# Performance work log

Hardware: AMD Instinct MI355X
Metric: run time of the kernel (lower is better)

## Reference

```python
import jax, jax.numpy as jnp
import numpy as np

EMB_SZ = 1024
NUM_HEADS = 16
HEAD_SIZE = EMB_SZ // NUM_HEADS  # 64; inputs must have last dim == HEAD_SIZE (module quirk)
B, S = 2, 2048


def setup_inputs() -> dict:
    key = jax.random.key(0)
    ks = jax.random.split(key, 8)
    return {
        "inputs_for_keys": jax.random.normal(ks[0], (B, S, HEAD_SIZE), jnp.float32),
        "inputs_for_values": jax.random.normal(ks[1], (B, S, HEAD_SIZE), jnp.float32),
        "inputs_for_queries": jax.random.normal(ks[2], (B, S, HEAD_SIZE), jnp.float32),
        # per-head projection weights, stacked over heads (glorot-ish scale)
        "Wk": jax.random.normal(ks[3], (NUM_HEADS, HEAD_SIZE, HEAD_SIZE), jnp.float32) * 0.125,
        "Wv": jax.random.normal(ks[4], (NUM_HEADS, HEAD_SIZE, HEAD_SIZE), jnp.float32) * 0.125,
        "Wq": jax.random.normal(ks[5], (NUM_HEADS, HEAD_SIZE, HEAD_SIZE), jnp.float32) * 0.125,
        "Wo": jax.random.normal(ks[6], (EMB_SZ, EMB_SZ), jnp.float32) * 0.03,
        "bo": jnp.zeros((EMB_SZ,), jnp.float32),
    }


def reference(inputs_for_keys, inputs_for_values, inputs_for_queries, Wk, Wv, Wq, Wo, bo):
    # Each head sees the SAME full inputs (module quirk), distinct weights per head.
    K = jnp.einsum('bsd,hde->bhse', inputs_for_keys, Wk)      # [B,H,Sk,hs]
    V = jnp.einsum('bsd,hde->bhse', inputs_for_values, Wv)    # [B,H,Sk,hs]
    Q = jnp.einsum('bsd,hde->bhse', inputs_for_queries, Wq)   # [B,H,Sq,hs]

    Sq, Sk = Q.shape[2], K.shape[2]
    scores = jnp.einsum('bhqe,bhke->bhqk', Q, K)              # [B,H,Sq,Sk]
    # causal additive mask: -inf strictly above the diagonal (as in np.triu(..., k=1))
    mask = jnp.triu(jnp.full((Sq, Sk), -jnp.inf, dtype=scores.dtype), k=1)
    scale = jnp.asarray(Sk, scores.dtype) ** 0.5
    # NOTE: original divides AFTER adding the mask; -inf/scale == -inf so math matches
    attn = jax.nn.softmax((scores + mask) / scale, axis=-1)   # [B,H,Sq,Sk]

    heads = jnp.einsum('bhqk,bhke->bhqe', attn, V)            # [B,H,Sq,hs]
    # concat heads along last dim (head order matches the Python-loop concat)
    concat = heads.transpose(0, 2, 1, 3).reshape(heads.shape[0], Sq, -1)  # [B,Sq,emb]
    return concat @ Wo + bo                                   # Dense(emb_sz), linear activation
```

## Files before the change

### kernel.cpp

```cpp
#include <hip/hip_runtime.h>
#include <hip/hip_bf16.h>
#include <cstdint>

typedef unsigned short u16;
typedef __bf16 bf16x8 __attribute__((ext_vector_type(8)));
typedef u16 u16x8 __attribute__((ext_vector_type(8)));
typedef unsigned u32x4 __attribute__((ext_vector_type(4)));
typedef float f32x4 __attribute__((ext_vector_type(4)));
typedef float f32x16 __attribute__((ext_vector_type(16)));

#define B_ 2
#define S_ 2048
#define H_ 16
#define HS_ 64
#define EMB_ 1024
#define QSCALE 0.022097086912079608f
#define LOG2E  1.4426950408889634f

static __device__ __forceinline__ u16 f2bf(float f) {
  unsigned int u = __float_as_uint(f);
  u += 0x7fffu + ((u >> 16) & 1u);
  return (u16)(u >> 16);
}

static __device__ __forceinline__ float ex2(float x) {
#if __has_builtin(__builtin_amdgcn_exp2f)
  return __builtin_amdgcn_exp2f(x);
#else
  float r; asm("v_exp_f32 %0, %1" : "=v"(r) : "v"(x)); return r;
#endif
}

static __device__ __forceinline__ f32x4 mfma16(u16x8 a, u16x8 b, f32x4 c) {
  return __builtin_amdgcn_mfma_f32_16x16x32_bf16(
      __builtin_bit_cast(bf16x8, a), __builtin_bit_cast(bf16x8, b), c, 0, 0, 0);
}
static __device__ __forceinline__ f32x16 mfma32(u16x8 a, u16x8 b, f32x16 c) {
  return __builtin_amdgcn_mfma_f32_32x32x16_bf16(
      __builtin_bit_cast(bf16x8, a), __builtin_bit_cast(bf16x8, b), c, 0, 0, 0);
}

static __device__ __forceinline__ char* swzb(void* base, int row, int colbyte) {
  return (char*)base + ((row * 128 + colbyte) ^ ((row & 7) << 4));
}
static __device__ __forceinline__ u16x8* swzp(void* base, int row, int colbyte) {
  return (u16x8*)swzb(base, row, colbyte);
}

static __device__ __forceinline__ void pk_swap(float a0, float a1, float b0, float b1,
                                               unsigned& x, unsigned& y) {
  unsigned A, Bv;
  asm("v_cvt_pk_bf16_f32 %0, %1, %2" : "=v"(A) : "v"(a0), "v"(a1));
  asm("v_cvt_pk_bf16_f32 %0, %1, %2" : "=v"(Bv) : "v"(b0), "v"(b1));
  asm("v_permlane32_swap_b32 %0, %1" : "+v"(A), "+v"(Bv));
  x = A; y = Bv;
}

__global__ __launch_bounds__(256) void k_transpose_wo(const float* __restrict__ Wo,
                                                      u16* __restrict__ Wot) {
  __shared__ __align__(16) u16 T[64][72];
  const int kb = blockIdx.y * 64, nb = blockIdx.x * 64;
  const int r = threadIdx.x >> 2;
  const int c0 = (threadIdx.x & 3) << 4;
  const float* src = Wo + (size_t)(kb + r) * EMB_ + nb + c0;
#pragma unroll
  for (int i = 0; i < 16; i += 4) {
    float4 f = *(const float4*)(src + i);
    T[c0 + i + 0][r] = f2bf(f.x);
    T[c0 + i + 1][r] = f2bf(f.y);
    T[c0 + i + 2][r] = f2bf(f.z);
    T[c0 + i + 3][r] = f2bf(f.w);
  }
  __syncthreads();
  u16* dst = Wot + (size_t)(nb + r) * EMB_ + kb + c0;
  *(u16x8*)(dst)     = *(const u16x8*)&T[r][c0];
  *(u16x8*)(dst + 8) = *(const u16x8*)&T[r][c0 + 8];
}

__global__ __launch_bounds__(256) void k_proj(
    const float* __restrict__ xq, const float* __restrict__ xk, const float* __restrict__ xv,
    const float* __restrict__ Wq, const float* __restrict__ Wk, const float* __restrict__ Wv,
    u16* __restrict__ Qf, u16* __restrict__ Kf, u16* __restrict__ Vf) {
  __shared__ __align__(16) u16 Xb[64][64];
  __shared__ __align__(16) u16 Wb[64][64];
  __shared__ __align__(16) u16 Tt[64][64];
  const int sb = blockIdx.x;
  const int bh = blockIdx.y;
  const int b = bh >> 4, h = bh & 15;
  const int t = threadIdx.x;
  const int r = t >> 2, c0 = (t & 3) << 4;
  const int lane = t & 63, wv = t >> 6;
  const int lq = lane & 15, lg = lane >> 4;
  const int l31 = lane & 31, hi = lane >> 5;
  const float* xs[3] = {xq, xk, xv};
  const float* ws3[3] = {Wq, Wk, Wv};

  for (int tn = 0; tn < 3; ++tn) {
    __syncthreads();
    const float* src = xs[tn] + ((size_t)(b * S_ + sb * 64 + r)) * HS_ + c0;
#pragma unroll
    for (int i = 0; i < 16; i += 8) {
      float4 fa = *(const float4*)(src + i);
      float4 fb = *(const float4*)(src + i + 4);
      u16x8 v = {f2bf(fa.x), f2bf(fa.y), f2bf(fa.z), f2bf(fa.w),
                 f2bf(fb.x), f2bf(fb.y), f2bf(fb.z), f2bf(fb.w)};
      *swzp(Xb, r, (c0 + i) * 2) = v;
    }
    const float* wsp = ws3[tn] + ((size_t)(h * HS_ + r)) * HS_ + c0;
#pragma unroll
    for (int i = 0; i < 16; i += 4) {
      float4 f = *(const float4*)(wsp + i);
      *(u16*)swzb(Wb, c0 + i + 0, r * 2) = f2bf(f.x);
      *(u16*)swzb(Wb, c0 + i + 1, r * 2) = f2bf(f.y);
      *(u16*)swzb(Wb, c0 + i + 2, r * 2) = f2bf(f.z);
      *(u16*)swzb(Wb, c0 + i + 3, r * 2) = f2bf(f.w);
    }
    __syncthreads();
    if (tn < 2) {
      u16x8 a0 = *swzp(Xb, wv * 16 + lq, lg * 16);
      u16x8 a1 = *swzp(Xb, wv * 16 + lq, 64 + lg * 16);
      const float osc = (tn == 0) ? (QSCALE * LOG2E) : 1.0f;
#pragma unroll
      for (int et = 0; et < 4; ++et) {
        u16x8 b0 = *swzp(Wb, et * 16 + lq, lg * 16);
        u16x8 b1 = *swzp(Wb, et * 16 + lq, 64 + lg * 16);
        f32x4 acc = {0.f, 0.f, 0.f, 0.f};
        acc = mfma16(a0, b0, acc);
        acc = mfma16(a1, b1, acc);
#pragma unroll
        for (int rr = 0; rr < 4; ++rr)
          *(u16*)swzb(Tt, wv * 16 + lg * 4 + rr, (et * 16 + lq) * 2) = f2bf(acc[rr] * osc);
      }
    } else {
      u16x8 xb0 = *swzp(Xb, wv * 16 + lq, lg * 16);
      u16x8 xb1 = *swzp(Xb, wv * 16 + lq, 64 + lg * 16);
#pragma unroll
      for (int et = 0; et < 4; ++et) {
        u16x8 a0 = *swzp(Wb, et * 16 + lq, lg * 16);
        u16x8 a1 = *swzp(Wb, et * 16 + lq, 64 + lg * 16);
        f32x4 acc = {0.f, 0.f, 0.f, 0.f};
        acc = mfma16(a0, xb0, acc);
        acc = mfma16(a1, xb1, acc);
#pragma unroll
        for (int rr = 0; rr < 4; ++rr)
          *(u16*)swzb(Tt, et * 16 + lg * 4 + rr, (wv * 16 + lq) * 2) = f2bf(acc[rr]);
      }
    }
    __syncthreads();
    if (tn < 2) {
      u16* dst = (tn == 0) ? Qf : Kf;
#pragma unroll
      for (int tl = 0; tl < 2; ++tl) {
        u16x8 v = *swzp(Tt, tl * 32 + l31, wv * 32 + hi * 16);
        size_t off = (((size_t)(bh * 64 + sb * 2 + tl)) * 4 + wv) * 512 + lane * 8;
        *(u16x8*)(dst + off) = v;
      }
    } else {
#pragma unroll
      for (int eta = 0; eta < 2; ++eta) {
        u16x8 v = *swzp(Tt, eta * 32 + l31, wv * 32 + hi * 16);
        size_t off = ((((size_t)(bh * 32 + sb)) * 2 + eta) * 4 + wv) * 512 + lane * 8;
        *(u16x8*)(Vf + off) = v;
      }
    }
  }
}

__global__ __launch_bounds__(128) void k_attn(
    const u16* __restrict__ Qf, const u16* __restrict__ Kf, const u16* __restrict__ Vf,
    u16* __restrict__ Co) {
  __shared__ float Xch[64][33];
  __shared__ __align__(16) u16 Osw[32][64];
  const int bid = blockIdx.x;
  const int xcd = bid & 7, idx = bid >> 3;
  const int bh = (xcd << 2) | (idx & 3);
  const int t = 63 - (idx >> 2);
  const int b = bh >> 4, h = bh & 15;
  const int w = threadIdx.x >> 6;
  const int l = threadIdx.x & 63;
  const int lq = l & 31, hi = l >> 5;
  const int qg = t * 32 + lq;
  const int n = (t >> 1) + 1;
  const int mid = n >> 1;
  const int jbeg = w ? mid : 0;
  const int jhot = w ? (n - 1) : mid;
  const float NEG = -3.0e38f;

  const u16* Qbase = Qf + (((size_t)(bh * 64 + t)) * 4) * 512 + l * 8;
  const u16* Kbase = Kf + ((size_t)(bh * 64) * 4) * 512 + l * 8;
  const u16* Vbase = Vf + ((size_t)(bh * 32) * 8) * 512 + l * 8;

  u16x8 qf[4];
#pragma unroll
  for (int ss = 0; ss < 4; ++ss) qf[ss] = *(const u16x8*)(Qbase + ss * 512);

  f32x16 o0, o1;
#pragma unroll
  for (int r = 0; r < 16; ++r) { o0[r] = 0.f; o1[r] = 0.f; }
  float ll = 0.f;

  u16x8 kl[4], kh[4], vl[4], vh[4];
  {
    const u16* p = Kbase + (size_t)jbeg * 8 * 512;
#pragma unroll
    for (int ss = 0; ss < 4; ++ss) {
      kl[ss] = *(const u16x8*)(p + ss * 512);
      kh[ss] = *(const u16x8*)(p + (4 + ss) * 512);
    }
  }

  for (int j = jbeg; j < jhot; ++j) {
    const u16* pv = Vbase + (size_t)j * 8 * 512;
#pragma unroll
    for (int kp = 0; kp < 4; ++kp) {
      vl[kp] = *(const u16x8*)(pv + kp * 512);
      vh[kp] = *(const u16x8*)(pv + (4 + kp) * 512);
    }
    f32x16 s0, s1;
#pragma unroll
    for (int r = 0; r < 16; ++r) { s0[r] = -16.f; s1[r] = -16.f; }
    __builtin_amdgcn_s_setprio(1);
    s0 = mfma32(kl[0], qf[0], s0);
    s0 = mfma32(kl[1], qf[1], s0);
    s0 = mfma32(kl[2], qf[2], s0);
    s0 = mfma32(kl[3], qf[3], s0);
    s1 = mfma32(kh[0], qf[0], s1);
    s1 = mfma32(kh[1], qf[1], s1);
    s1 = mfma32(kh[2], qf[2], s1);
    s1 = mfma32(kh[3], qf[3], s1);
    __builtin_amdgcn_s_setprio(0);
    {
      const u16* pk = Kbase + (size_t)(j + 1) * 8 * 512;
#pragma unroll
      for (int ss = 0; ss < 4; ++ss) {
        kl[ss] = *(const u16x8*)(pk + ss * 512);
        kh[ss] = *(const u16x8*)(pk + (4 + ss) * 512);
      }
    }
    float ps = 0.f;
#pragma unroll
    for (int r = 0; r < 16; ++r) { s0[r] = ex2(s0[r]); ps += s0[r]; }
#pragma unroll
    for (int r = 0; r < 16; ++r) { s1[r] = ex2(s1[r]); ps += s1[r]; }
    ll += ps;
    u16x8 pf0, pf1, pf2, pf3;
    {
      unsigned w0, w1, w2, w3;
      pk_swap(s0[0], s0[1], s0[4], s0[5], w0, w2);
      pk_swap(s0[2], s0[3], s0[6], s0[7], w1, w3);
      pf0 = __builtin_bit_cast(u16x8, (u32x4){w0, w1, w2, w3});
      pk_swap(s0[8], s0[9], s0[12], s0[13], w0, w2);
      pk_swap(s0[10], s0[11], s0[14], s0[15], w1, w3);
      pf1 = __builtin_bit_cast(u16x8, (u32x4){w0, w1, w2, w3});
      pk_swap(s1[0], s1[1], s1[4], s1[5], w0, w2);
      pk_swap(s1[2], s1[3], s1[6], s1[7], w1, w3);
      pf2 = __builtin_bit_cast(u16x8, (u32x4){w0, w1, w2, w3});
      pk_swap(s1[8], s1[9], s1[12], s1[13], w0, w2);
      pk_swap(s1[10], s1[11], s1[14], s1[15], w1, w3);
      pf3 = __builtin_bit_cast(u16x8, (u32x4){w0, w1, w2, w3});
    }
    __builtin_amdgcn_s_setprio(1);
    o0 = mfma32(vl[0], pf0, o0);
    o1 = mfma32(vh[0], pf0, o1);
    o0 = mfma32(vl[1], pf1, o0);
    o1 = mfma32(vh[1], pf1, o1);
    o0 = mfma32(vl[2], pf2, o0);
    o1 = mfma32(vh[2], pf2, o1);
    o0 = mfma32(vl[3], pf3, o0);
    o1 = mfma32(vh[3], pf3, o1);
    __builtin_amdgcn_s_setprio(0);
  }

  if (w) {
    const int j = n - 1;
    const u16* pv = Vbase + (size_t)j * 8 * 512;
#pragma unroll
    for (int kp = 0; kp < 4; ++kp) {
      vl[kp] = *(const u16x8*)(pv + kp * 512);
      vh[kp] = *(const u16x8*)(pv + (4 + kp) * 512);
    }
    f32x16 s0, s1;
#pragma unroll
    for (int r = 0; r < 16; ++r) { s0[r] = -16.f; s1[r] = -16.f; }
    s0 = mfma32(kl[0], qf[0], s0);
    s0 = mfma32(kl[1], qf[1], s0);
    s0 = mfma32(kl[2], qf[2], s0);
    s0 = mfma32(kl[3], qf[3], s0);
    if (t & 1) {
      s1 = mfma32(kh[0], qf[0], s1);
      s1 = mfma32(kh[1], qf[1], s1);
      s1 = mfma32(kh[2], qf[2], s1);
      s1 = mfma32(kh[3], qf[3], s1);
    }
    if (t & 1) {
#pragma unroll
      for (int r = 0; r < 16; ++r) {
        int kv = j * 64 + 32 + (r & 3) + 8 * (r >> 2) + 4 * hi;
        if (kv > qg) s1[r] = NEG;
      }
    } else {
#pragma unroll
      for (int r = 0; r < 16; ++r) {
        int kv = j * 64 + (r & 3) + 8 * (r >> 2) + 4 * hi;
        if (kv > qg) s0[r] = NEG;
      }
    }
    float ps = 0.f;
#pragma unroll
    for (int r = 0; r < 16; ++r) { s0[r] = ex2(s0[r]); ps += s0[r]; }
    if (t & 1) {
#pragma unroll
      for (int r = 0; r < 16; ++r) { s1[r] = ex2(s1[r]); ps += s1[r]; }
    }
    ll += ps;
    u16x8 pf0, pf1, pf2, pf3;
    {
      unsigned w0, w1, w2, w3;
      pk_swap(s0[0], s0[1], s0[4], s0[5], w0, w2);
      pk_swap(s0[2], s0[3], s0[6], s0[7], w1, w3);
      pf0 = __builtin_bit_cast(u16x8, (u32x4){w0, w1, w2, w3});
      pk_swap(s0[8], s0[9], s0[12], s0[13], w0, w2);
      pk_swap(s0[10], s0[11], s0[14], s0[15], w1, w3);
      pf1 = __builtin_bit_cast(u16x8, (u32x4){w0, w1, w2, w3});
      if (t & 1) {
        pk_swap(s1[0], s1[1], s1[4], s1[5], w0, w2);
        pk_swap(s1[2], s1[3], s1[6], s1[7], w1, w3);
        pf2 = __builtin_bit_cast(u16x8, (u32x4){w0, w1, w2, w3});
        pk_swap(s1[8], s1[9], s1[12], s1[13], w0, w2);
        pk_swap(s1[10], s1[11], s1[14], s1[15], w1, w3);
        pf3 = __builtin_bit_cast(u16x8, (u32x4){w0, w1, w2, w3});
      }
    }
    o0 = mfma32(vl[0], pf0, o0);
    o1 = mfma32(vh[0], pf0, o1);
    o0 = mfma32(vl[1], pf1, o0);
    o1 = mfma32(vh[1], pf1, o1);
    if (t & 1) {
      o0 = mfma32(vl[2], pf2, o0);
      o1 = mfma32(vh[2], pf2, o1);
      o0 = mfma32(vl[3], pf3, o0);
      o1 = mfma32(vh[3], pf3, o1);
    }
#pragma unroll
    for (int r = 0; r < 16; ++r) { Xch[l][r] = o0[r]; Xch[l][16 + r] = o1[r]; }
    Xch[l][32] = ll;
  }
  __syncthreads();
  if (w == 0) {
#pragma unroll
    for (int r = 0; r < 16; ++r) { o0[r] += Xch[l][r]; o1[r] += Xch[l][16 + r]; }
    ll += Xch[l][32];
    ll += __shfl_xor(ll, 32);
    float inv = 1.0f / ll;
#pragma unroll
    for (int r = 0; r < 16; ++r) {
      int drow = (r & 3) + 8 * (r >> 2) + 4 * hi;
      *(u16*)swzb(Osw, lq, drow * 2) = f2bf(o0[r] * inv);
      *(u16*)swzb(Osw, lq, (32 + drow) * 2) = f2bf(o1[r] * inv);
    }
    u16* dst = Co + ((size_t)(b * S_ + qg)) * EMB_ + h * HS_ + hi * 32;
#pragma unroll
    for (int k = 0; k < 4; ++k) {
      u16x8 vv = *swzp(Osw, lq, (hi * 32 + k * 8) * 2);
      *(u16x8*)(dst + k * 8) = vv;
    }
  }
}

__global__ __launch_bounds__(256) void k_outproj(
    const u16* __restrict__ Cc, const u16* __restrict__ Wot,
    const float* __restrict__ bo, float* __restrict__ out) {
  __shared__ __align__(16) u16 As[64][64];
  __shared__ __align__(16) u16 Bs[128][64];
  const int bid = blockIdx.x;
  const int xcd = bid & 7, sl = bid >> 3;
  const int mb = (xcd << 3) | (sl >> 3);
  const int nb = sl & 7;
  const int t = threadIdx.x;
  const int lane = t & 63, wv = t >> 6;
  const int lq = lane & 15, lg = lane >> 4;
  const int wr = wv >> 1, wc = wv & 1;
  const int srA = t >> 2, scA = (t & 3) << 4;
  const int srB = t >> 1, scB = (t & 1) << 5;
  f32x4 acc[2][4];
#pragma unroll
  for (int mi = 0; mi < 2; ++mi)
#pragma unroll
    for (int ni = 0; ni < 4; ++ni) { f32x4 z = {0.f, 0.f, 0.f, 0.f}; acc[mi][ni] = z; }
  const u16* abase = Cc + ((size_t)(mb * 64 + srA)) * EMB_ + scA;
  const u16* bbase = Wot + ((size_t)(nb * 128 + srB)) * EMB_ + scB;
  u16x8 ar[2], br[4];
#pragma unroll
  for (int q = 0; q < 2; ++q) ar[q] = *(const u16x8*)(abase + q * 8);
#pragma unroll
  for (int q = 0; q < 4; ++q) br[q] = *(const u16x8*)(bbase + q * 8);
  for (int kt = 0; kt < 16; ++kt) {
    __syncthreads();
#pragma unroll
    for (int q = 0; q < 2; ++q) *swzp(As, srA, (scA + q * 8) * 2) = ar[q];
#pragma unroll
    for (int q = 0; q < 4; ++q) *swzp(Bs, srB, (scB + q * 8) * 2) = br[q];
    __syncthreads();
    if (kt < 15) {
#pragma unroll
      for (int q = 0; q < 2; ++q) ar[q] = *(const u16x8*)(abase + (kt + 1) * 64 + q * 8);
#pragma unroll
      for (int q = 0; q < 4; ++q) br[q] = *(const u16x8*)(bbase + (kt + 1) * 64 + q * 8);
    }
#pragma unroll
    for (int kf = 0; kf < 2; ++kf) {
      u16x8 af[2], bf[4];
#pragma unroll
      for (int mi = 0; mi < 2; ++mi)
        af[mi] = *swzp(As, wr * 32 + mi * 16 + lq, kf * 64 + lg * 16);
#pragma unroll
      for (int ni = 0; ni < 4; ++ni)
        bf[ni] = *swzp(Bs, wc * 64 + ni * 16 + lq, kf * 64 + lg * 16);
#pragma unroll
      for (int mi = 0; mi < 2; ++mi)
#pragma unroll
        for (int ni = 0; ni < 4; ++ni)
          acc[mi][ni] = mfma16(af[mi], bf[ni], acc[mi][ni]);
    }
  }
#pragma unroll
  for (int mi = 0; mi < 2; ++mi) {
#pragma unroll
    for (int ni = 0; ni < 4; ++ni) {
      int col = nb * 128 + wc * 64 + ni * 16 + lq;
      float bv = bo[col];
#pragma unroll
      for (int rr = 0; rr < 4; ++rr) {
        int row = mb * 64 + wr * 32 + mi * 16 + lg * 4 + rr;
        out[(size_t)row * EMB_ + col] = acc[mi][ni][rr] + bv;
      }
    }
  }
}

extern "C" void kernel_launch(void* const* d_in, const int* in_sizes, int n_in,
                              void* d_out, int out_size, void* d_ws, size_t ws_size,
                              hipStream_t stream) {
  const float* xk = (const float*)d_in[0];
  const float* xv = (const float*)d_in[1];
  const float* xq = (const float*)d_in[2];
  const float* Wk = (const float*)d_in[3];
  const float* Wv = (const float*)d_in[4];
  const float* Wq = (const float*)d_in[5];
  const float* Wo = (const float*)d_in[6];
  const float* bo = (const float*)d_in[7];
  float* out = (float*)d_out;
  char* ws = (char*)d_ws;
  const size_t MB8 = (size_t)8 * 1024 * 1024;
  u16* Qfw = (u16*)(ws);
  u16* Kfw = (u16*)(ws + MB8);
  u16* Vfw = (u16*)(ws + 2 * MB8);
  u16* Cw  = (u16*)(ws + 3 * MB8);
  u16* Wot = (u16*)(ws + 4 * MB8);

  k_transpose_wo<<<dim3(16, 16), 256, 0, stream>>>(Wo, Wot);
  k_proj<<<dim3(32, 32), 256, 0, stream>>>(xq, xk, xv, Wq, Wk, Wv, Qfw, Kfw, Vfw);
  k_attn<<<2048, 128, 0, stream>>>(Qfw, Kfw, Vfw, Cw);
  k_outproj<<<512, 256, 0, stream>>>(Cw, Wot, bo, out);
}
```

Before: 71.73 us.

## Pair causal query tiles per attention block, split projection grid, prefetch V

The projection kernel now spreads Q, K and V over a third grid dimension, so it runs one tensor per block instead of looping over three. The attention kernel processes two query tiles per block (t and 63-t) to balance causal work, and halves the grid. It also prefetches V one step ahead alongside K, uses a tree reduction for the row sums, and adds a launch-bounds occupancy hint. Costs are more register pressure from the V double-buffering, and a longer serial run per block.

After: 65.34 us. 8.9% less time.

```diff
diff --git a/kernel.cpp b/kernel.cpp
--- a/kernel.cpp
+++ b/kernel.cpp
@@ -29,6 +29,16 @@
 #else
   float r; asm("v_exp_f32 %0, %1" : "=v"(r) : "v"(x)); return r;
 #endif
+}
+
+static __device__ __forceinline__ float tsum16(const f32x16& s) {
+  float a0 = s[0] + s[1],  a1 = s[2] + s[3];
+  float a2 = s[4] + s[5],  a3 = s[6] + s[7];
+  float a4 = s[8] + s[9],  a5 = s[10] + s[11];
+  float a6 = s[12] + s[13], a7 = s[14] + s[15];
+  a0 += a1; a2 += a3; a4 += a5; a6 += a7;
+  a0 += a2; a4 += a6;
+  return a0 + a4;
 }
 
 static __device__ __forceinline__ f32x4 mfma16(u16x8 a, u16x8 b, f32x4 c) {
@@ -86,87 +96,85 @@
   __shared__ __align__(16) u16 Tt[64][64];
   const int sb = blockIdx.x;
   const int bh = blockIdx.y;
+  const int tn = blockIdx.z;
   const int b = bh >> 4, h = bh & 15;
   const int t = threadIdx.x;
   const int r = t >> 2, c0 = (t & 3) << 4;
   const int lane = t & 63, wv = t >> 6;
   const int lq = lane & 15, lg = lane >> 4;
   const int l31 = lane & 31, hi = lane >> 5;
-  const float* xs[3] = {xq, xk, xv};
-  const float* ws3[3] = {Wq, Wk, Wv};
-
-  for (int tn = 0; tn < 3; ++tn) {
-    __syncthreads();
-    const float* src = xs[tn] + ((size_t)(b * S_ + sb * 64 + r)) * HS_ + c0;
-#pragma unroll
-    for (int i = 0; i < 16; i += 8) {
-      float4 fa = *(const float4*)(src + i);
-      float4 fb = *(const float4*)(src + i + 4);
-      u16x8 v = {f2bf(fa.x), f2bf(fa.y), f2bf(fa.z), f2bf(fa.w),
-                 f2bf(fb.x), f2bf(fb.y), f2bf(fb.z), f2bf(fb.w)};
-      *swzp(Xb, r, (c0 + i) * 2) = v;
-    }
-    const float* wsp = ws3[tn] + ((size_t)(h * HS_ + r)) * HS_ + c0;
-#pragma unroll
-    for (int i = 0; i < 16; i += 4) {
-      float4 f = *(const float4*)(wsp + i);
-      *(u16*)swzb(Wb, c0 + i + 0, r * 2) = f2bf(f.x);
-      *(u16*)swzb(Wb, c0 + i + 1, r * 2) = f2bf(f.y);
-      *(u16*)swzb(Wb, c0 + i + 2, r * 2) = f2bf(f.z);
-      *(u16*)swzb(Wb, c0 + i + 3, r * 2) = f2bf(f.w);
-    }
-    __syncthreads();
-    if (tn < 2) {
-      u16x8 a0 = *swzp(Xb, wv * 16 + lq, lg * 16);
-      u16x8 a1 = *swzp(Xb, wv * 16 + lq, 64 + lg * 16);
-      const float osc = (tn == 0) ? (QSCALE * LOG2E) : 1.0f;
-#pragma unroll
-      for (int et = 0; et < 4; ++et) {
-        u16x8 b0 = *swzp(Wb, et * 16 + lq, lg * 16);
-        u16x8 b1 = *swzp(Wb, et * 16 + lq, 64 + lg * 16);
-        f32x4 acc = {0.f, 0.f, 0.f, 0.f};
-        acc = mfma16(a0, b0, acc);
-        acc = mfma16(a1, b1, acc);
-#pragma unroll
-        for (int rr = 0; rr < 4; ++rr)
-          *(u16*)swzb(Tt, wv * 16 + lg * 4 + rr, (et * 16 + lq) * 2) = f2bf(acc[rr] * osc);
-      }
-    } else {
-      u16x8 xb0 = *swzp(Xb, wv * 16 + lq, lg * 16);
-      u16x8 xb1 = *swzp(Xb, wv * 16 + lq, 64 + lg * 16);
-#pragma unroll
-      for (int et = 0; et < 4; ++et) {
-        u16x8 a0 = *swzp(Wb, et * 16 + lq, lg * 16);
-        u16x8 a1 = *swzp(Wb, et * 16 + lq, 64 + lg * 16);
-        f32x4 acc = {0.f, 0.f, 0.f, 0.f};
-        acc = mfma16(a0, xb0, acc);
-        acc = mfma16(a1, xb1, acc);
-#pragma unroll
-        for (int rr = 0; rr < 4; ++rr)
-          *(u16*)swzb(Tt, et * 16 + lg * 4 + rr, (wv * 16 + lq) * 2) = f2bf(acc[rr]);
-      }
-    }
-    __syncthreads();
-    if (tn < 2) {
-      u16* dst = (tn == 0) ? Qf : Kf;
-#pragma unroll
-      for (int tl = 0; tl < 2; ++tl) {
-        u16x8 v = *swzp(Tt, tl * 32 + l31, wv * 32 + hi * 16);
-        size_t off = (((size_t)(bh * 64 + sb * 2 + tl)) * 4 + wv) * 512 + lane * 8;
-        *(u16x8*)(dst + off) = v;
-      }
-    } else {
-#pragma unroll
-      for (int eta = 0; eta < 2; ++eta) {
-        u16x8 v = *swzp(Tt, eta * 32 + l31, wv * 32 + hi * 16);
-        size_t off = ((((size_t)(bh * 32 + sb)) * 2 + eta) * 4 + wv) * 512 + lane * 8;
-        *(u16x8*)(Vf + off) = v;
-      }
-    }
-  }
-}
-
-__global__ __launch_bounds__(128) void k_attn(
+  const float* xs = (tn == 0) ? xq : (tn == 1) ? xk : xv;
+  const float* wsp3 = (tn == 0) ? Wq : (tn == 1) ? Wk : Wv;
+
+  const float* src = xs + ((size_t)(b * S_ + sb * 64 + r)) * HS_ + c0;
+#pragma unroll
+  for (int i = 0; i < 16; i += 8) {
+    float4 fa = *(const float4*)(src + i);
+    float4 fb = *(const float4*)(src + i + 4);
+    u16x8 v = {f2bf(fa.x), f2bf(fa.y), f2bf(fa.z), f2bf(fa.w),
+               f2bf(fb.x), f2bf(fb.y), f2bf(fb.z), f2bf(fb.w)};
+    *swzp(Xb, r, (c0 + i) * 2) = v;
+  }
+  const float* wsp = wsp3 + ((size_t)(h * HS_ + r)) * HS_ + c0;
+#pragma unroll
+  for (int i = 0; i < 16; i += 4) {
+    float4 f = *(const float4*)(wsp + i);
+    *(u16*)swzb(Wb, c0 + i + 0, r * 2) = f2bf(f.x);
+    *(u16*)swzb(Wb, c0 + i + 1, r * 2) = f2bf(f.y);
+    *(u16*)swzb(Wb, c0 + i + 2, r * 2) = f2bf(f.z);
+    *(u16*)swzb(Wb, c0 + i + 3, r * 2) = f2bf(f.w);
+  }
+  __syncthreads();
+  if (tn < 2) {
+    u16x8 a0 = *swzp(Xb, wv * 16 + lq, lg * 16);
+    u16x8 a1 = *swzp(Xb, wv * 16 + lq, 64 + lg * 16);
+    const float osc = (tn == 0) ? (QSCALE * LOG2E) : 1.0f;
+#pragma unroll
+    for (int et = 0; et < 4; ++et) {
+      u16x8 b0 = *swzp(Wb, et * 16 + lq, lg * 16);
+      u16x8 b1 = *swzp(Wb, et * 16 + lq, 64 + lg * 16);
+      f32x4 acc = {0.f, 0.f, 0.f, 0.f};
+      acc = mfma16(a0, b0, acc);
+      acc = mfma16(a1, b1, acc);
+#pragma unroll
+      for (int rr = 0; rr < 4; ++rr)
+        *(u16*)swzb(Tt, wv * 16 + lg * 4 + rr, (et * 16 + lq) * 2) = f2bf(acc[rr] * osc);
+    }
+  } else {
+    u16x8 xb0 = *swzp(Xb, wv * 16 + lq, lg * 16);
+    u16x8 xb1 = *swzp(Xb, wv * 16 + lq, 64 + lg * 16);
+#pragma unroll
+    for (int et = 0; et < 4; ++et) {
+      u16x8 a0 = *swzp(Wb, et * 16 + lq, lg * 16);
+      u16x8 a1 = *swzp(Wb, et * 16 + lq, 64 + lg * 16);
+      f32x4 acc = {0.f, 0.f, 0.f, 0.f};
+      acc = mfma16(a0, xb0, acc);
+      acc = mfma16(a1, xb1, acc);
+#pragma unroll
+      for (int rr = 0; rr < 4; ++rr)
+        *(u16*)swzb(Tt, et * 16 + lg * 4 + rr, (wv * 16 + lq) * 2) = f2bf(acc[rr]);
+    }
+  }
+  __syncthreads();
+  if (tn < 2) {
+    u16* dst = (tn == 0) ? Qf : Kf;
+#pragma unroll
+    for (int tl = 0; tl < 2; ++tl) {
+      u16x8 v = *swzp(Tt, tl * 32 + l31, wv * 32 + hi * 16);
+      size_t off = (((size_t)(bh * 64 + sb * 2 + tl)) * 4 + wv) * 512 + lane * 8;
+      *(u16x8*)(dst + off) = v;
+    }
+  } else {
+#pragma unroll
+    for (int eta = 0; eta < 2; ++eta) {
+      u16x8 v = *swzp(Tt, eta * 32 + l31, wv * 32 + hi * 16);
+      size_t off = ((((size_t)(bh * 32 + sb)) * 2 + eta) * 4 + wv) * 512 + lane * 8;
+      *(u16x8*)(Vf + off) = v;
+    }
+  }
+}
+
+__global__ __launch_bounds__(128, 2) void k_attn(
     const u16* __restrict__ Qf, const u16* __restrict__ Kf, const u16* __restrict__ Vf,
     u16* __restrict__ Co) {
   __shared__ float Xch[64][33];
@@ -174,155 +182,83 @@
   const int bid = blockIdx.x;
   const int xcd = bid & 7, idx = bid >> 3;
   const int bh = (xcd << 2) | (idx & 3);
-  const int t = 63 - (idx >> 2);
+  const int pr = idx >> 2;
   const int b = bh >> 4, h = bh & 15;
   const int w = threadIdx.x >> 6;
   const int l = threadIdx.x & 63;
   const int lq = l & 31, hi = l >> 5;
-  const int qg = t * 32 + lq;
-  const int n = (t >> 1) + 1;
-  const int mid = n >> 1;
-  const int jbeg = w ? mid : 0;
-  const int jhot = w ? (n - 1) : mid;
   const float NEG = -3.0e38f;
 
-  const u16* Qbase = Qf + (((size_t)(bh * 64 + t)) * 4) * 512 + l * 8;
   const u16* Kbase = Kf + ((size_t)(bh * 64) * 4) * 512 + l * 8;
   const u16* Vbase = Vf + ((size_t)(bh * 32) * 8) * 512 + l * 8;
 
-  u16x8 qf[4];
-#pragma unroll
-  for (int ss = 0; ss < 4; ++ss) qf[ss] = *(const u16x8*)(Qbase + ss * 512);
-
-  f32x16 o0, o1;
-#pragma unroll
-  for (int r = 0; r < 16; ++r) { o0[r] = 0.f; o1[r] = 0.f; }
-  float ll = 0.f;
-
-  u16x8 kl[4], kh[4], vl[4], vh[4];
-  {
-    const u16* p = Kbase + (size_t)jbeg * 8 * 512;
-#pragma unroll
-    for (int ss = 0; ss < 4; ++ss) {
-      kl[ss] = *(const u16x8*)(p + ss * 512);
-      kh[ss] = *(const u16x8*)(p + (4 + ss) * 512);
-    }
-  }
-
-  for (int j = jbeg; j < jhot; ++j) {
-    const u16* pv = Vbase + (size_t)j * 8 * 512;
-#pragma unroll
-    for (int kp = 0; kp < 4; ++kp) {
-      vl[kp] = *(const u16x8*)(pv + kp * 512);
-      vh[kp] = *(const u16x8*)(pv + (4 + kp) * 512);
-    }
-    f32x16 s0, s1;
-#pragma unroll
-    for (int r = 0; r < 16; ++r) { s0[r] = -16.f; s1[r] = -16.f; }
-    __builtin_amdgcn_s_setprio(1);
-    s0 = mfma32(kl[0], qf[0], s0);
-    s0 = mfma32(kl[1], qf[1], s0);
-    s0 = mfma32(kl[2], qf[2], s0);
-    s0 = mfma32(kl[3], qf[3], s0);
-    s1 = mfma32(kh[0], qf[0], s1);
-    s1 = mfma32(kh[1], qf[1], s1);
-    s1 = mfma32(kh[2], qf[2], s1);
-    s1 = mfma32(kh[3], qf[3], s1);
-    __builtin_amdgcn_s_setprio(0);
+#pragma unroll 1
+  for (int ph = 0; ph < 2; ++ph) {
+    const int t = ph ? (63 - pr) : pr;
+    const int qg = t * 32 + lq;
+    const int n = (t >> 1) + 1;
+    const int mid = n >> 1;
+    const int jbeg = w ? mid : 0;
+    const int jhot = w ? (n - 1) : mid;
+
+    const u16* Qbase = Qf + (((size_t)(bh * 64 + t)) * 4) * 512 + l * 8;
+    u16x8 qf[4];
+#pragma unroll
+    for (int ss = 0; ss < 4; ++ss) qf[ss] = *(const u16x8*)(Qbase + ss * 512);
+
+    f32x16 o0, o1;
+#pragma unroll
+    for (int r = 0; r < 16; ++r) { o0[r] = 0.f; o1[r] = 0.f; }
+    float ll = 0.f;
+
+    u16x8 kl[4], kh[4], vl[4], vh[4];
     {
-      const u16* pk = Kbase + (size_t)(j + 1) * 8 * 512;
+      const u16* pk = Kbase + (size_t)jbeg * 8 * 512;
+      const u16* pv = Vbase + (size_t)jbeg * 8 * 512;
 #pragma unroll
       for (int ss = 0; ss < 4; ++ss) {
         kl[ss] = *(const u16x8*)(pk + ss * 512);
         kh[ss] = *(const u16x8*)(pk + (4 + ss) * 512);
-      }
-    }
-    float ps = 0.f;
-#pragma unroll
-    for (int r = 0; r < 16; ++r) { s0[r] = ex2(s0[r]); ps += s0[r]; }
-#pragma unroll
-    for (int r = 0; r < 16; ++r) { s1[r] = ex2(s1[r]); ps += s1[r]; }
-    ll += ps;
-    u16x8 pf0, pf1, pf2, pf3;
-    {
-      unsigned w0, w1, w2, w3;
-      pk_swap(s0[0], s0[1], s0[4], s0[5], w0, w2);
-      pk_swap(s0[2], s0[3], s0[6], s0[7], w1, w3);
-      pf0 = __builtin_bit_cast(u16x8, (u32x4){w0, w1, w2, w3});
-      pk_swap(s0[8], s0[9], s0[12], s0[13], w0, w2);
-      pk_swap(s0[10], s0[11], s0[14], s0[15], w1, w3);
-      pf1 = __builtin_bit_cast(u16x8, (u32x4){w0, w1, w2, w3});
-      pk_swap(s1[0], s1[1], s1[4], s1[5], w0, w2);
-      pk_swap(s1[2], s1[3], s1[6], s1[7], w1, w3);
-      pf2 = __builtin_bit_cast(u16x8, (u32x4){w0, w1, w2, w3});
-      pk_swap(s1[8], s1[9], s1[12], s1[13], w0, w2);
-      pk_swap(s1[10], s1[11], s1[14], s1[15], w1, w3);
-      pf3 = __builtin_bit_cast(u16x8, (u32x4){w0, w1, w2, w3});
-    }
-    __builtin_amdgcn_s_setprio(1);
-    o0 = mfma32(vl[0], pf0, o0);
-    o1 = mfma32(vh[0], pf0, o1);
-    o0 = mfma32(vl[1], pf1, o0);
-    o1 = mfma32(vh[1], pf1, o1);
-    o0 = mfma32(vl[2], pf2, o0);
-    o1 = mfma32(vh[2], pf2, o1);
-    o0 = mfma32(vl[3], pf3, o0);
-    o1 = mfma32(vh[3], pf3, o1);
-    __builtin_amdgcn_s_setprio(0);
-  }
-
-  if (w) {
-    const int j = n - 1;
-    const u16* pv = Vbase + (size_t)j * 8 * 512;
-#pragma unroll
-    for (int kp = 0; kp < 4; ++kp) {
-      vl[kp] = *(const u16x8*)(pv + kp * 512);
-      vh[kp] = *(const u16x8*)(pv + (4 + kp) * 512);
-    }
-    f32x16 s0, s1;
-#pragma unroll
-    for (int r = 0; r < 16; ++r) { s0[r] = -16.f; s1[r] = -16.f; }
-    s0 = mfma32(kl[0], qf[0], s0);
-    s0 = mfma32(kl[1], qf[1], s0);
-    s0 = mfma32(kl[2], qf[2], s0);
-    s0 = mfma32(kl[3], qf[3], s0);
-    if (t & 1) {
+        vl[ss] = *(const u16x8*)(pv + ss * 512);
+        vh[ss] = *(const u16x8*)(pv + (4 + ss) * 512);
+      }
+    }
+
+    for (int j = jbeg; j < jhot; ++j) {
+      f32x16 s0, s1;
+#pragma unroll
+      for (int r = 0; r < 16; ++r) { s0[r] = -16.f; s1[r] = -16.f; }
+      __builtin_amdgcn_s_setprio(1);
+      s0 = mfma32(kl[0], qf[0], s0);
+      s0 = mfma32(kl[1], qf[1], s0);
+      s0 = mfma32(kl[2], qf[2], s0);
+      s0 = mfma32(kl[3], qf[3], s0);
       s1 = mfma32(kh[0], qf[0], s1);
       s1 = mfma32(kh[1], qf[1], s1);
       s1 = mfma32(kh[2], qf[2], s1);
       s1 = mfma32(kh[3], qf[3], s1);
-    }
-    if (t & 1) {
-#pragma unroll
-      for (int r = 0; r < 16; ++r) {
-        int kv = j * 64 + 32 + (r & 3) + 8 * (r >> 2) + 4 * hi;
-        if (kv > qg) s1[r] = NEG;
-      }
-    } else {
-#pragma unroll
-      for (int r = 0; r < 16; ++r) {
-        int kv = j * 64 + (r & 3) + 8 * (r >> 2) + 4 * hi;
-        if (kv > qg) s0[r] = NEG;
-      }
-    }
-    float ps = 0.f;
-#pragma unroll
-    for (int r = 0; r < 16; ++r) { s0[r] = ex2(s0[r]); ps += s0[r]; }
-    if (t & 1) {
-#pragma unroll
-      for (int r = 0; r < 16; ++r) { s1[r] = ex2(s1[r]); ps += s1[r]; }
-    }
-    ll += ps;
-    u16x8 pf0, pf1, pf2, pf3;
-    {
-      unsigned w0, w1, w2, w3;
-      pk_swap(s0[0], s0[1], s0[4], s0[5], w0, w2);
-      pk_swap(s0[2], s0[3], s0[6], s0[7], w1, w3);
-      pf0 = __builtin_bit_cast(u16x8, (u32x4){w0, w1, w2, w3});
-      pk_swap(s0[8], s0[9], s0[12], s0[13], w0, w2);
-      pk_swap(s0[10], s0[11], s0[14], s0[15], w1, w3);
-      pf1 = __builtin_bit_cast(u16x8, (u32x4){w0, w1, w2, w3});
-      if (t & 1) {
+      __builtin_amdgcn_s_setprio(0);
+      {
+        const u16* pk = Kbase + (size_t)(j + 1) * 8 * 512;
+#pragma unroll
+        for (int ss = 0; ss < 4; ++ss) {
+          kl[ss] = *(const u16x8*)(pk + ss * 512);
+          kh[ss] = *(const u16x8*)(pk + (4 + ss) * 512);
+        }
+      }
+#pragma unroll
+      for (int r = 0; r < 16; ++r) s0[r] = ex2(s0[r]);
+#pragma unroll
+      for (int r = 0; r < 16; ++r) s1[r] = ex2(s1[r]);
+      u16x8 pf0, pf1, pf2, pf3;
+      {
+        unsigned w0, w1, w2, w3;
+        pk_swap(s0[0], s0[1], s0[4], s0[5], w0, w2);
+        pk_swap(s0[2], s0[3], s0[6], s0[7], w1, w3);
+        pf0 = __builtin_bit_cast(u16x8, (u32x4){w0, w1, w2, w3});
+        pk_swap(s0[8], s0[9], s0[12], s0[13], w0, w2);
+        pk_swap(s0[10], s0[11], s0[14], s0[15], w1, w3);
+        pf1 = __builtin_bit_cast(u16x8, (u32x4){w0, w1, w2, w3});
         pk_swap(s1[0], s1[1], s1[4], s1[5], w0, w2);
         pk_swap(s1[2], s1[3], s1[6], s1[7], w1, w3);
         pf2 = __builtin_bit_cast(u16x8, (u32x4){w0, w1, w2, w3});
@@ -330,40 +266,116 @@
         pk_swap(s1[10], s1[11], s1[14], s1[15], w1, w3);
         pf3 = __builtin_bit_cast(u16x8, (u32x4){w0, w1, w2, w3});
       }
-    }
-    o0 = mfma32(vl[0], pf0, o0);
-    o1 = mfma32(vh[0], pf0, o1);
-    o0 = mfma32(vl[1], pf1, o0);
-    o1 = mfma32(vh[1], pf1, o1);
-    if (t & 1) {
+      __builtin_amdgcn_s_setprio(1);
+      o0 = mfma32(vl[0], pf0, o0);
+      o1 = mfma32(vh[0], pf0, o1);
+      o0 = mfma32(vl[1], pf1, o0);
+      o1 = mfma32(vh[1], pf1, o1);
       o0 = mfma32(vl[2], pf2, o0);
       o1 = mfma32(vh[2], pf2, o1);
       o0 = mfma32(vl[3], pf3, o0);
       o1 = mfma32(vh[3], pf3, o1);
-    }
-#pragma unroll
-    for (int r = 0; r < 16; ++r) { Xch[l][r] = o0[r]; Xch[l][16 + r] = o1[r]; }
-    Xch[l][32] = ll;
-  }
-  __syncthreads();
-  if (w == 0) {
-#pragma unroll
-    for (int r = 0; r < 16; ++r) { o0[r] += Xch[l][r]; o1[r] += Xch[l][16 + r]; }
-    ll += Xch[l][32];
-    ll += __shfl_xor(ll, 32);
-    float inv = 1.0f / ll;
-#pragma unroll
-    for (int r = 0; r < 16; ++r) {
-      int drow = (r & 3) + 8 * (r >> 2) + 4 * hi;
-      *(u16*)swzb(Osw, lq, drow * 2) = f2bf(o0[r] * inv);
-      *(u16*)swzb(Osw, lq, (32 + drow) * 2) = f2bf(o1[r] * inv);
-    }
-    u16* dst = Co + ((size_t)(b * S_ + qg)) * EMB_ + h * HS_ + hi * 32;
-#pragma unroll
-    for (int k = 0; k < 4; ++k) {
-      u16x8 vv = *swzp(Osw, lq, (hi * 32 + k * 8) * 2);
-      *(u16x8*)(dst + k * 8) = vv;
-    }
+      __builtin_amdgcn_s_setprio(0);
+      {
+        const u16* pv = Vbase + (size_t)(j + 1) * 8 * 512;
+#pragma unroll
+        for (int ss = 0; ss < 4; ++ss) {
+          vl[ss] = *(const u16x8*)(pv + ss * 512);
+          vh[ss] = *(const u16x8*)(pv + (4 + ss) * 512);
+        }
+      }
+      ll += tsum16(s0) + tsum16(s1);
+    }
+
+    if (w) {
+      const int j = n - 1;
+      f32x16 s0, s1;
+#pragma unroll
+      for (int r = 0; r < 16; ++r) { s0[r] = -16.f; s1[r] = -16.f; }
+      s0 = mfma32(kl[0], qf[0], s0);
+      s0 = mfma32(kl[1], qf[1], s0);
+      s0 = mfma32(kl[2], qf[2], s0);
+      s0 = mfma32(kl[3], qf[3], s0);
+      if (t & 1) {
+        s1 = mfma32(kh[0], qf[0], s1);
+        s1 = mfma32(kh[1], qf[1], s1);
+        s1 = mfma32(kh[2], qf[2], s1);
+        s1 = mfma32(kh[3], qf[3], s1);
+      }
+      if (t & 1) {
+#pragma unroll
+        for (int r = 0; r < 16; ++r) {
+          int kv = j * 64 + 32 + (r & 3) + 8 * (r >> 2) + 4 * hi;
+          if (kv > qg) s1[r] = NEG;
+        }
+      } else {
+#pragma unroll
+        for (int r = 0; r < 16; ++r) {
+          int kv = j * 64 + (r & 3) + 8 * (r >> 2) + 4 * hi;
+          if (kv > qg) s0[r] = NEG;
+        }
+      }
+#pragma unroll
+      for (int r = 0; r < 16; ++r) s0[r] = ex2(s0[r]);
+      ll += tsum16(s0);
+      if (t & 1) {
+#pragma unroll
+        for (int r = 0; r < 16; ++r) s1[r] = ex2(s1[r]);
+        ll += tsum16(s1);
+      }
+      u16x8 pf0, pf1, pf2, pf3;
+      {
+        unsigned w0, w1, w2, w3;
+        pk_swap(s0[0], s0[1], s0[4], s0[5], w0, w2);
+        pk_swap(s0[2], s0[3], s0[6], s0[7], w1, w3);
+        pf0 = __builtin_bit_cast(u16x8, (u32x4){w0, w1, w2, w3});
+        pk_swap(s0[8], s0[9], s0[12], s0[13], w0, w2);
+        pk_swap(s0[10], s0[11], s0[14], s0[15], w1, w3);
+        pf1 = __builtin_bit_cast(u16x8, (u32x4){w0, w1, w2, w3});
+        if (t & 1) {
+          pk_swap(s1[0], s1[1], s1[4], s1[5], w0, w2);
+          pk_swap(s1[2], s1[3], s1[6], s1[7], w1, w3);
+          pf2 = __builtin_bit_cast(u16x8, (u32x4){w0, w1, w2, w3});
+          pk_swap(s1[8], s1[9], s1[12], s1[13], w0, w2);
+          pk_swap(s1[10], s1[11], s1[14], s1[15], w1, w3);
+          pf3 = __builtin_bit_cast(u16x8, (u32x4){w0, w1, w2, w3});
+        }
+      }
+      o0 = mfma32(vl[0], pf0, o0);
+      o1 = mfma32(vh[0], pf0, o1);
+      o0 = mfma32(vl[1], pf1, o0);
+      o1 = mfma32(vh[1], pf1, o1);
+      if (t & 1) {
+        o0 = mfma32(vl[2], pf2, o0);
+        o1 = mfma32(vh[2], pf2, o1);
+        o0 = mfma32(vl[3], pf3, o0);
+        o1 = mfma32(vh[3], pf3, o1);
+      }
+#pragma unroll
+      for (int r = 0; r < 16; ++r) { Xch[l][r] = o0[r]; Xch[l][16 + r] = o1[r]; }
+      Xch[l][32] = ll;
+    }
+    __syncthreads();
+    if (w == 0) {
+#pragma unroll
+      for (int r = 0; r < 16; ++r) { o0[r] += Xch[l][r]; o1[r] += Xch[l][16 + r]; }
+      ll += Xch[l][32];
+      ll += __shfl_xor(ll, 32);
+      float inv = 1.0f / ll;
+#pragma unroll
+      for (int r = 0; r < 16; ++r) {
+        int drow = (r & 3) + 8 * (r >> 2) + 4 * hi;
+        *(u16*)swzb(Osw, lq, drow * 2) = f2bf(o0[r] * inv);
+        *(u16*)swzb(Osw, lq, (32 + drow) * 2) = f2bf(o1[r] * inv);
+      }
+      u16* dst = Co + ((size_t)(b * S_ + qg)) * EMB_ + h * HS_ + hi * 32;
+#pragma unroll
+      for (int k = 0; k < 4; ++k) {
+        u16x8 vv = *swzp(Osw, lq, (hi * 32 + k * 8) * 2);
+        *(u16x8*)(dst + k * 8) = vv;
+      }
+    }
+    __syncthreads();
   }
 }
 
@@ -459,7 +471,7 @@
   u16* Wot = (u16*)(ws + 4 * MB8);
 
   k_transpose_wo<<<dim3(16, 16), 256, 0, stream>>>(Wo, Wot);
-  k_proj<<<dim3(32, 32), 256, 0, stream>>>(xq, xk, xv, Wq, Wk, Wv, Qfw, Kfw, Vfw);
-  k_attn<<<2048, 128, 0, stream>>>(Qfw, Kfw, Vfw, Cw);
+  k_proj<<<dim3(32, 32, 3), 256, 0, stream>>>(xq, xk, xv, Wq, Wk, Wv, Qfw, Kfw, Vfw);
+  k_attn<<<1024, 128, 0, stream>>>(Qfw, Kfw, Vfw, Cw);
   k_outproj<<<512, 256, 0, stream>>>(Cw, Wot, bo, out);
 }
```
